# Optimization experiments

Hardware: AMD Instinct MI355X
Metric: run time of the kernel (lower is better)

Reference implementation:

```python
import jax, jax.numpy as jnp
from jax import lax
import numpy as np

T, B, DIN, NQ = 256, 2048, 128, 16  # hidden_dim == n_qubits (required by module math)


def setup_inputs() -> dict:
    key = jax.random.key(0)
    k1, k2, k3 = jax.random.split(key, 3)
    inputs = jax.random.normal(k1, (T, B, DIN), dtype=jnp.float32)
    # stacked params for the 4 gates: forget, input, update, output
    W = jax.random.normal(k2, (4, NQ, DIN + NQ), dtype=jnp.float32) * 0.1
    b = jnp.zeros((4, NQ), dtype=jnp.float32)
    theta = jax.random.normal(k3, (4, NQ), dtype=jnp.float32)
    return {"inputs": inputs, "W": W, "b": b, "theta": theta}


def reference(inputs, W, b, theta):
    # Analytic simulation of each QGate circuit:
    #   RX(x_i) then RX(theta_i) on wire i  ->  product state, <Z_i> = cos(x_i + theta_i)
    #   CNOT chain (0->1, 1->2, ...): Heisenberg picture maps Z_k -> Z_0 Z_1 ... Z_k,
    Tn, Bn, _ = inputs.shape
    nq = theta.shape[-1]
    h0 = jnp.zeros((Bn, nq), dtype=inputs.dtype)
    c0 = jnp.zeros((Bn, nq), dtype=inputs.dtype)

    def step(carry, x):
        hx, cx = carry
        combined = jnp.concatenate([x, hx], axis=1)              # [B, Din+H]
        z = jnp.einsum('bd,gnd->bgn', combined, W) + b           # [B, 4, nq]
        q = jnp.cumprod(jnp.cos(z + theta), axis=-1)             # quantum gate expectations
        f = jax.nn.sigmoid(q[:, 0])
        i = jax.nn.sigmoid(q[:, 1])
        g = jnp.tanh(q[:, 2])
        o = jax.nn.sigmoid(q[:, 3])
        cx = f * cx + i * g
        hx = o * jnp.tanh(cx)
        return (hx, cx), hx

    (hx, cx), outputs = lax.scan(step, (h0, c0), inputs)
    return outputs, hx, cx
```

## Files before the change

kernel.cpp:

```cpp
#include <hip/hip_runtime.h>
#include <hip/hip_bf16.h>
#include <stdint.h>


#define T_STEPS 256
#define BATCH   2048
#define DIN     128
#define NQ      16
#define LCOLS   64
#define DTOT    144
#define NCH     64
#define CH_XSTRIDE ((size_t)4 * BATCH * DIN)

typedef __attribute__((ext_vector_type(8))) short bf16x8;
typedef __attribute__((ext_vector_type(4))) float f32x4;

__device__ __forceinline__ float bf2f(unsigned short u) {
    union { unsigned int i; float f; } v; v.i = ((unsigned int)u) << 16; return v.f;
}
__device__ __forceinline__ unsigned short f2bf(float f) {
    union { float f; unsigned int i; } v; v.f = f;
    unsigned int i = v.i;
    unsigned int r = i + 0x7fffu + ((i >> 16) & 1u);
    return (unsigned short)(r >> 16);
}
__device__ __forceinline__ float ldval(const float* p) { return *p; }
__device__ __forceinline__ float ldval(const unsigned short* p) { return bf2f(*p); }

__device__ __forceinline__ int detect_bf16(const unsigned int* __restrict__ xw, int lane) {
    int cnt = 0;
#pragma unroll
    for (int i = 0; i < 4; ++i) {
        unsigned int w = xw[lane + i * 64];
        unsigned int e = (w >> 7) & 0xFFu;
        cnt += (e >= 100u && e <= 140u) ? 1 : 0;
    }
#pragma unroll
    for (int d = 32; d > 0; d >>= 1) cnt += __shfl_down(cnt, d, 64);
    int tot = __shfl(cnt, 0, 64);
    return (tot >= 140) ? 1 : 0;
}

template <int CTRL>
__device__ __forceinline__ float dpp_sh(float v) {
    int r = __builtin_amdgcn_update_dpp(__builtin_bit_cast(int, 1.0f),
                                        __builtin_bit_cast(int, v),
                                        CTRL, 0xF, 0xF, false);
    return __builtin_bit_cast(float, r);
}
template <int CTRL>
__device__ __forceinline__ float rot16(float v) {
    int r = __builtin_amdgcn_update_dpp(0, __builtin_bit_cast(int, v),
                                        CTRL, 0xF, 0xF, false);
    return __builtin_bit_cast(float, r);
}

template <int BASE>
__device__ __forceinline__ void qstep(int t, int g, int n, float cur,
                                      const float (&Wp)[16], float& h, float& c,
                                      float& hsave, float* __restrict__ out, int b,
                                      int a_f, int a_i, int a_g, int a_o)
{
    float h1  = rot16<0x121>(h), h2  = rot16<0x122>(h), h3  = rot16<0x123>(h);
    float h4  = rot16<0x124>(h), h5  = rot16<0x125>(h), h6  = rot16<0x126>(h), h7  = rot16<0x127>(h);
    float h8  = rot16<0x128>(h), h9  = rot16<0x129>(h), h10 = rot16<0x12A>(h), h11 = rot16<0x12B>(h);
    float h12 = rot16<0x12C>(h), h13 = rot16<0x12D>(h), h14 = rot16<0x12E>(h), h15 = rot16<0x12F>(h);

    float s0 = fmaf(Wp[0],  h,   fmaf(Wp[1],  h1,  fmaf(Wp[2],  h2,  Wp[3]  * h3)));
    float s1 = fmaf(Wp[4],  h4,  fmaf(Wp[5],  h5,  fmaf(Wp[6],  h6,  Wp[7]  * h7)));
    float s2 = fmaf(Wp[8],  h8,  fmaf(Wp[9],  h9,  fmaf(Wp[10], h10, Wp[11] * h11)));
    float s3 = fmaf(Wp[12], h12, fmaf(Wp[13], h13, fmaf(Wp[14], h14, Wp[15] * h15)));
    float z = cur + ((s0 + s1) + (s2 + s3));

    float cz = __cosf(z);
    cz *= dpp_sh<BASE + 1>(cz);
    cz *= dpp_sh<BASE + 2>(cz);
    cz *= dpp_sh<BASE + 4>(cz);
    cz *= dpp_sh<BASE + 8>(cz);

    float a = (g == 2) ? 2.f * cz : cz;
    float e = __expf(-a);
    float rr = __builtin_amdgcn_rcpf(1.f + e);
    float s = (g == 2) ? (1.f - e) * rr : rr;

    int si = __builtin_bit_cast(int, s);
    float fv = __builtin_bit_cast(float, __builtin_amdgcn_ds_bpermute(a_f, si));
    float iv = __builtin_bit_cast(float, __builtin_amdgcn_ds_bpermute(a_i, si));
    float gv = __builtin_bit_cast(float, __builtin_amdgcn_ds_bpermute(a_g, si));
    float ov = __builtin_bit_cast(float, __builtin_amdgcn_ds_bpermute(a_o, si));

    c = fmaf(fv, c, iv * gv);
    float e2 = __expf(-2.f * c);
    float tc = (1.f - e2) * __builtin_amdgcn_rcpf(1.f + e2);
    h = ov * tc;

    if ((t & 3) == g) hsave = h;
    if ((t & 3) == 3)
        out[(size_t)(t - 3 + g) * (BATCH * NQ) + (size_t)b * NQ + n] = hsave;
}

template <int BASE, typename InT>
__device__ __forceinline__ void fused_main(
    const InT* __restrict__ x, const InT* __restrict__ W,
    const InT* __restrict__ bv, const InT* __restrict__ th,
    float* __restrict__ out, int b0, int w, int lane,
    const float (&Wp)[16], float (*zbuf)[16][64], bf16x8* __restrict__ xshv)
{
    const int m = lane & 15, quad = lane >> 4;
    const int g = quad, n = m;
    const int b = b0 + w;
    const int a_f = n << 2, a_i = (16 + n) << 2, a_g = (32 + n) << 2, a_o = (48 + n) << 2;

    bf16x8 bh[4], bl[4];
    if constexpr (sizeof(InT) == 2) {
#pragma unroll
        for (int kt = 0; kt < 4; ++kt)
            bh[kt] = *(const bf16x8*)((const unsigned short*)W +
                                      (size_t)(w * 16 + m) * DTOT + kt * 32 + quad * 8);
    } else {
#pragma unroll
        for (int kt = 0; kt < 4; ++kt) {
            const float* p = (const float*)W + (size_t)(w * 16 + m) * DTOT + kt * 32 + quad * 8;
#pragma unroll
            for (int j = 0; j < 8; ++j) {
                float wv = p[j];
                unsigned short hh = f2bf(wv);
                bh[kt][j] = (short)hh;
                bl[kt][j] = (short)f2bf(wv - bf2f(hh));
            }
        }
    }
    const float bias = ldval(bv + lane) + ldval(th + lane);

    const InT* xbase = x + ((size_t)(m >> 2) * BATCH + (size_t)(b0 + (m & 3))) * DIN
                         + w * 32 + quad * 8;

    bf16x8* xw0 = xshv + (((m * 4 + w) * 4 + quad) * 2);

    f32x4 rx0, rx1; bf16x8 rbx;
    auto LOAD = [&](int ch) {
        const InT* p = xbase + (size_t)ch * CH_XSTRIDE;
        if constexpr (sizeof(InT) == 2) {
            rbx = *(const bf16x8*)p;
        } else {
            rx0 = *(const f32x4*)p;
            rx1 = *(const f32x4*)((const float*)p + 4);
        }
    };
    auto PRODUCE = [&](int ch) {
        if constexpr (sizeof(InT) == 2) {
            xw0[0] = rbx;
        } else {
            bf16x8 ah, al;
#pragma unroll
            for (int j = 0; j < 4; ++j) {
                float xv = rx0[j];
                unsigned short hh = f2bf(xv);
                ah[j] = (short)hh; al[j] = (short)f2bf(xv - bf2f(hh));
            }
#pragma unroll
            for (int j = 0; j < 4; ++j) {
                float xv = rx1[j];
                unsigned short hh = f2bf(xv);
                ah[4 + j] = (short)hh; al[4 + j] = (short)f2bf(xv - bf2f(hh));
            }
            xw0[0] = ah; xw0[1] = al;
        }
        __syncthreads();
        f32x4 acc = {};
#pragma unroll
        for (int kt = 0; kt < 4; ++kt) {
            const bf16x8 ah = xshv[((m * 4 + kt) * 4 + quad) * 2];
            if constexpr (sizeof(InT) == 2) {
                acc = __builtin_amdgcn_mfma_f32_16x16x32_bf16(ah, bh[kt], acc, 0, 0, 0);
            } else {
                const bf16x8 al = xshv[((m * 4 + kt) * 4 + quad) * 2 + 1];
                acc = __builtin_amdgcn_mfma_f32_16x16x32_bf16(ah, bh[kt], acc, 0, 0, 0);
                acc = __builtin_amdgcn_mfma_f32_16x16x32_bf16(al, bh[kt], acc, 0, 0, 0);
                acc = __builtin_amdgcn_mfma_f32_16x16x32_bf16(ah, bl[kt], acc, 0, 0, 0);
            }
        }
        const int buf = ch & 1;
#pragma unroll
        for (int r = 0; r < 4; ++r)
            zbuf[buf][quad * 4 + r][w * 16 + m] = acc[r];
        __syncthreads();
    };

    float h = 0.f, c = 0.f, hsave = 0.f;

    LOAD(0);
    PRODUCE(0);
    LOAD(1);

    for (int ch = 0; ch < NCH; ++ch) {
        float zr[4];
#pragma unroll
        for (int dt = 0; dt < 4; ++dt)
            zr[dt] = zbuf[ch & 1][dt * 4 + w][lane] + bias;
        if (ch < NCH - 1) {
            PRODUCE(ch + 1);
            if (ch + 2 < NCH) LOAD(ch + 2);
        }
#pragma unroll
        for (int dt = 0; dt < 4; ++dt)
            qstep<BASE>(ch * 4 + dt, g, n, zr[dt], Wp, h, c, hsave, out, b,
                        a_f, a_i, a_g, a_o);
    }

    if (g == 0) {
        out[(size_t)T_STEPS * BATCH * NQ + (size_t)b * NQ + n] = h;
        out[(size_t)T_STEPS * BATCH * NQ + (size_t)BATCH * NQ + (size_t)b * NQ + n] = c;
    }
}

__global__ __launch_bounds__(256) void qlstm_fused(
    const void* __restrict__ x_, const void* __restrict__ W_,
    const void* __restrict__ b_, const void* __restrict__ th_,
    float* __restrict__ out)
{
    __shared__ float zbuf[2][16][64];
    __shared__ bf16x8 xshv[512];

    const int lane = threadIdx.x & 63;
    const int w    = threadIdx.x >> 6;
    const int b0   = blockIdx.x * 4;
    const int n    = lane & 15;

    const int isbf = __builtin_amdgcn_readfirstlane(detect_bf16((const unsigned int*)x_, lane));

    int pr  = __builtin_amdgcn_update_dpp(0, lane, 0x121, 0xF, 0xF, false);
    int p0r = __shfl(pr, 0, 64);
    const int d = (p0r == 1) ? 1 : 15;

    float Wp[16];
    if (isbf) {
        const unsigned short* W = (const unsigned short*)W_;
#pragma unroll
        for (int k = 0; k < 16; ++k)
            Wp[k] = bf2f(W[(size_t)lane * DTOT + DIN + ((n + k * d) & 15)]);
    } else {
        const float* W = (const float*)W_;
#pragma unroll
        for (int k = 0; k < 16; ++k)
            Wp[k] = W[(size_t)lane * DTOT + DIN + ((n + k * d) & 15)];
    }

    int probe = __builtin_amdgcn_update_dpp(999, lane, 0x111, 0xF, 0xF, false);
    int p2 = __shfl(probe, 2, 64);

    if (isbf) {
        if (p2 == 1) fused_main<0x110, unsigned short>((const unsigned short*)x_, (const unsigned short*)W_,
                                                       (const unsigned short*)b_, (const unsigned short*)th_,
                                                       out, b0, w, lane, Wp, zbuf, xshv);
        else         fused_main<0x100, unsigned short>((const unsigned short*)x_, (const unsigned short*)W_,
                                                       (const unsigned short*)b_, (const unsigned short*)th_,
                                                       out, b0, w, lane, Wp, zbuf, xshv);
    } else {
        if (p2 == 1) fused_main<0x110, float>((const float*)x_, (const float*)W_,
                                              (const float*)b_, (const float*)th_,
                                              out, b0, w, lane, Wp, zbuf, xshv);
        else         fused_main<0x100, float>((const float*)x_, (const float*)W_,
                                              (const float*)b_, (const float*)th_,
                                              out, b0, w, lane, Wp, zbuf, xshv);
    }
}

extern "C" void kernel_launch(void* const* d_in, const int* in_sizes, int n_in,
                              void* d_out, int out_size, void* d_ws, size_t ws_size,
                              hipStream_t stream) {
    const void* x  = d_in[0];
    const void* W  = d_in[1];
    const void* bv = d_in[2];
    const void* th = d_in[3];
    (void)d_ws; (void)ws_size;
    qlstm_fused<<<BATCH / 4, 256, 0, stream>>>(x, W, bv, th, (float*)d_out);
}
```

Before: 441.7 us.

## Make each wave compute its own 16-step input projection tile without block barriers

Each wave now handles one batch element over 16 timesteps and computes the full 64-column input projection for that tile itself, using 4x4 register-resident weight fragments. Per-wave shared buffers with padded rows replace the block-wide shared staging, so the two __syncthreads per chunk go away. On targets that support it, the gate-value gather uses permlane16/32 swaps instead of four ds_bpermute ops. The cost is much higher register pressure (16 weight fragments, plus low parts for fp32 inputs), and launch bounds now request 2 blocks per CU.

```diff
diff --git a/kernel.cpp b/kernel.cpp
--- a/kernel.cpp
+++ b/kernel.cpp
@@ -9,11 +9,21 @@
 #define NQ      16
 #define LCOLS   64
 #define DTOT    144
-#define NCH     64
-#define CH_XSTRIDE ((size_t)4 * BATCH * DIN)
+#define NTILE   16
+#define ZROW    68
 
 typedef __attribute__((ext_vector_type(8))) short bf16x8;
 typedef __attribute__((ext_vector_type(4))) float f32x4;
+typedef __attribute__((ext_vector_type(2))) int   int2v;
+
+#if defined(__has_builtin)
+#if __has_builtin(__builtin_amdgcn_permlane16_swap) && __has_builtin(__builtin_amdgcn_permlane32_swap)
+#define USE_PLSWAP 1
+#endif
+#endif
+#ifndef USE_PLSWAP
+#define USE_PLSWAP 0
+#endif
 
 __device__ __forceinline__ float bf2f(unsigned short u) {
     union { unsigned int i; float f; } v; v.i = ((unsigned int)u) << 16; return v.f;
@@ -59,6 +69,7 @@
 __device__ __forceinline__ void qstep(int t, int g, int n, float cur,
                                       const float (&Wp)[16], float& h, float& c,
                                       float& hsave, float* __restrict__ out, int b,
+                                      bool m0, bool m1,
                                       int a_f, int a_i, int a_g, int a_o)
 {
     float h1  = rot16<0x121>(h), h2  = rot16<0x122>(h), h3  = rot16<0x123>(h);
@@ -83,15 +94,38 @@
     float rr = __builtin_amdgcn_rcpf(1.f + e);
     float s = (g == 2) ? (1.f - e) * rr : rr;
 
+    float fv, iv, gv, ov;
+#if USE_PLSWAP
     int si = __builtin_bit_cast(int, s);
-    float fv = __builtin_bit_cast(float, __builtin_amdgcn_ds_bpermute(a_f, si));
-    float iv = __builtin_bit_cast(float, __builtin_amdgcn_ds_bpermute(a_i, si));
-    float gv = __builtin_bit_cast(float, __builtin_amdgcn_ds_bpermute(a_g, si));
-    float ov = __builtin_bit_cast(float, __builtin_amdgcn_ds_bpermute(a_o, si));
+    int2v e1 = __builtin_amdgcn_permlane16_swap(si, si, false, false);
+    int c1i = m0 ? e1[0] : e1[1];
+    int2v e2 = __builtin_amdgcn_permlane32_swap(si, si, false, false);
+    int c2i = m1 ? e2[0] : e2[1];
+    int2v e3 = __builtin_amdgcn_permlane16_swap(c2i, c2i, false, false);
+    int c3i = m0 ? e3[0] : e3[1];
+    float C0 = s;
+    float C1 = __builtin_bit_cast(float, c1i);
+    float C2 = __builtin_bit_cast(float, c2i);
+    float C3 = __builtin_bit_cast(float, c3i);
+    float P  = m1 ? C2 : C0;
+    float Q  = m1 ? C3 : C1;
+    float R_ = m1 ? C0 : C2;
+    float S_ = m1 ? C1 : C3;
+    fv = m0 ? Q  : P;
+    iv = m0 ? P  : Q;
+    gv = m0 ? S_ : R_;
+    ov = m0 ? R_ : S_;
+#else
+    int si = __builtin_bit_cast(int, s);
+    fv = __builtin_bit_cast(float, __builtin_amdgcn_ds_bpermute(a_f, si));
+    iv = __builtin_bit_cast(float, __builtin_amdgcn_ds_bpermute(a_i, si));
+    gv = __builtin_bit_cast(float, __builtin_amdgcn_ds_bpermute(a_g, si));
+    ov = __builtin_bit_cast(float, __builtin_amdgcn_ds_bpermute(a_o, si));
+#endif
 
     c = fmaf(fv, c, iv * gv);
-    float e2 = __expf(-2.f * c);
-    float tc = (1.f - e2) * __builtin_amdgcn_rcpf(1.f + e2);
+    float e2t = __expf(-2.f * c);
+    float tc = (1.f - e2t) * __builtin_amdgcn_rcpf(1.f + e2t);
     h = ov * tc;
 
     if ((t & 3) == g) hsave = h;
@@ -103,88 +137,88 @@
 __device__ __forceinline__ void fused_main(
     const InT* __restrict__ x, const InT* __restrict__ W,
     const InT* __restrict__ bv, const InT* __restrict__ th,
-    float* __restrict__ out, int b0, int w, int lane,
-    const float (&Wp)[16], float (*zbuf)[16][64], bf16x8* __restrict__ xshv)
+    float* __restrict__ out, int b, int lane,
+    const float (&Wp)[16], float (*zt)[16][ZROW])
 {
     const int m = lane & 15, quad = lane >> 4;
     const int g = quad, n = m;
-    const int b = b0 + w;
+    const bool m0 = (g & 1) != 0, m1 = (g & 2) != 0;
     const int a_f = n << 2, a_i = (16 + n) << 2, a_g = (32 + n) << 2, a_o = (48 + n) << 2;
 
-    bf16x8 bh[4], bl[4];
+    bf16x8 bh[4][4], bl[4][4];
     if constexpr (sizeof(InT) == 2) {
 #pragma unroll
         for (int kt = 0; kt < 4; ++kt)
-            bh[kt] = *(const bf16x8*)((const unsigned short*)W +
-                                      (size_t)(w * 16 + m) * DTOT + kt * 32 + quad * 8);
+#pragma unroll
+            for (int nb = 0; nb < 4; ++nb)
+                bh[kt][nb] = *(const bf16x8*)((const unsigned short*)W +
+                             (size_t)(nb * 16 + m) * DTOT + kt * 32 + quad * 8);
     } else {
 #pragma unroll
+        for (int kt = 0; kt < 4; ++kt)
+#pragma unroll
+            for (int nb = 0; nb < 4; ++nb) {
+                const float* p = (const float*)W + (size_t)(nb * 16 + m) * DTOT + kt * 32 + quad * 8;
+#pragma unroll
+                for (int j = 0; j < 8; ++j) {
+                    float wv = p[j];
+                    unsigned short hh = f2bf(wv);
+                    bh[kt][nb][j] = (short)hh;
+                    bl[kt][nb][j] = (short)f2bf(wv - bf2f(hh));
+                }
+            }
+    }
+    const float bias = ldval(bv + lane) + ldval(th + lane);
+
+    const InT* xbase = x + ((size_t)m * BATCH + (size_t)b) * DIN + quad * 8;
+
+    f32x4 rx[8]; bf16x8 rbx[4];
+    auto LOAD = [&](int tl) {
+        const InT* p = xbase + (size_t)tl * ((size_t)16 * BATCH * DIN);
+#pragma unroll
         for (int kt = 0; kt < 4; ++kt) {
-            const float* p = (const float*)W + (size_t)(w * 16 + m) * DTOT + kt * 32 + quad * 8;
-#pragma unroll
-            for (int j = 0; j < 8; ++j) {
-                float wv = p[j];
-                unsigned short hh = f2bf(wv);
-                bh[kt][j] = (short)hh;
-                bl[kt][j] = (short)f2bf(wv - bf2f(hh));
+            if constexpr (sizeof(InT) == 2) {
+                rbx[kt] = *(const bf16x8*)(p + kt * 32);
+            } else {
+                rx[2 * kt]     = *(const f32x4*)((const float*)p + kt * 32);
+                rx[2 * kt + 1] = *(const f32x4*)((const float*)p + kt * 32 + 4);
             }
         }
-    }
-    const float bias = ldval(bv + lane) + ldval(th + lane);
-
-    const InT* xbase = x + ((size_t)(m >> 2) * BATCH + (size_t)(b0 + (m & 3))) * DIN
-                         + w * 32 + quad * 8;
-
-    bf16x8* xw0 = xshv + (((m * 4 + w) * 4 + quad) * 2);
-
-    f32x4 rx0, rx1; bf16x8 rbx;
-    auto LOAD = [&](int ch) {
-        const InT* p = xbase + (size_t)ch * CH_XSTRIDE;
-        if constexpr (sizeof(InT) == 2) {
-            rbx = *(const bf16x8*)p;
-        } else {
-            rx0 = *(const f32x4*)p;
-            rx1 = *(const f32x4*)((const float*)p + 4);
-        }
     };
-    auto PRODUCE = [&](int ch) {
-        if constexpr (sizeof(InT) == 2) {
-            xw0[0] = rbx;
-        } else {
-            bf16x8 ah, al;
-#pragma unroll
-            for (int j = 0; j < 4; ++j) {
-                float xv = rx0[j];
-                unsigned short hh = f2bf(xv);
-                ah[j] = (short)hh; al[j] = (short)f2bf(xv - bf2f(hh));
-            }
-#pragma unroll
-            for (int j = 0; j < 4; ++j) {
-                float xv = rx1[j];
-                unsigned short hh = f2bf(xv);
-                ah[4 + j] = (short)hh; al[4 + j] = (short)f2bf(xv - bf2f(hh));
-            }
-            xw0[0] = ah; xw0[1] = al;
-        }
-        __syncthreads();
-        f32x4 acc = {};
+    auto PRODUCE = [&](int tl) {
+        f32x4 acc[4] = {};
 #pragma unroll
         for (int kt = 0; kt < 4; ++kt) {
-            const bf16x8 ah = xshv[((m * 4 + kt) * 4 + quad) * 2];
             if constexpr (sizeof(InT) == 2) {
-                acc = __builtin_amdgcn_mfma_f32_16x16x32_bf16(ah, bh[kt], acc, 0, 0, 0);
+#pragma unroll
+                for (int nb = 0; nb < 4; ++nb)
+                    acc[nb] = __builtin_amdgcn_mfma_f32_16x16x32_bf16(rbx[kt], bh[kt][nb], acc[nb], 0, 0, 0);
             } else {
-                const bf16x8 al = xshv[((m * 4 + kt) * 4 + quad) * 2 + 1];
-                acc = __builtin_amdgcn_mfma_f32_16x16x32_bf16(ah, bh[kt], acc, 0, 0, 0);
-                acc = __builtin_amdgcn_mfma_f32_16x16x32_bf16(al, bh[kt], acc, 0, 0, 0);
-                acc = __builtin_amdgcn_mfma_f32_16x16x32_bf16(ah, bl[kt], acc, 0, 0, 0);
+                bf16x8 ah, al;
+#pragma unroll
+                for (int j = 0; j < 8; ++j) {
+                    float xv = rx[2 * kt + (j >> 2)][j & 3];
+                    unsigned short hh = f2bf(xv);
+                    ah[j] = (short)hh;
+                    al[j] = (short)f2bf(xv - bf2f(hh));
+                }
+#pragma unroll
+                for (int nb = 0; nb < 4; ++nb)
+                    acc[nb] = __builtin_amdgcn_mfma_f32_16x16x32_bf16(ah, bh[kt][nb], acc[nb], 0, 0, 0);
+#pragma unroll
+                for (int nb = 0; nb < 4; ++nb)
+                    acc[nb] = __builtin_amdgcn_mfma_f32_16x16x32_bf16(al, bh[kt][nb], acc[nb], 0, 0, 0);
+#pragma unroll
+                for (int nb = 0; nb < 4; ++nb)
+                    acc[nb] = __builtin_amdgcn_mfma_f32_16x16x32_bf16(ah, bl[kt][nb], acc[nb], 0, 0, 0);
             }
         }
-        const int buf = ch & 1;
-#pragma unroll
-        for (int r = 0; r < 4; ++r)
-            zbuf[buf][quad * 4 + r][w * 16 + m] = acc[r];
-        __syncthreads();
+        const int buf = tl & 1;
+#pragma unroll
+        for (int nb = 0; nb < 4; ++nb)
+#pragma unroll
+            for (int r = 0; r < 4; ++r)
+                zt[buf][quad * 4 + r][nb * 16 + m] = acc[nb][r];
     };
 
     float h = 0.f, c = 0.f, hsave = 0.f;
@@ -193,19 +227,26 @@
     PRODUCE(0);
     LOAD(1);
 
-    for (int ch = 0; ch < NCH; ++ch) {
-        float zr[4];
-#pragma unroll
-        for (int dt = 0; dt < 4; ++dt)
-            zr[dt] = zbuf[ch & 1][dt * 4 + w][lane] + bias;
-        if (ch < NCH - 1) {
-            PRODUCE(ch + 1);
-            if (ch + 2 < NCH) LOAD(ch + 2);
-        }
-#pragma unroll
-        for (int dt = 0; dt < 4; ++dt)
-            qstep<BASE>(ch * 4 + dt, g, n, zr[dt], Wp, h, c, hsave, out, b,
-                        a_f, a_i, a_g, a_o);
+#pragma unroll 1
+    for (int tl = 0; tl < NTILE; ++tl) {
+        const int buf = tl & 1;
+        const int t0 = tl * 16;
+        float zr0[8], zr1[8];
+#pragma unroll
+        for (int j = 0; j < 8; ++j) zr0[j] = zt[buf][j][lane] + bias;
+        if (tl < NTILE - 1) PRODUCE(tl + 1);
+        if (tl < NTILE - 2) LOAD(tl + 2);
+#pragma unroll
+        for (int j = 0; j < 4; ++j)
+            qstep<BASE>(t0 + j, g, n, zr0[j], Wp, h, c, hsave, out, b, m0, m1, a_f, a_i, a_g, a_o);
+#pragma unroll
+        for (int j = 0; j < 8; ++j) zr1[j] = zt[buf][8 + j][lane] + bias;
+#pragma unroll
+        for (int j = 4; j < 8; ++j)
+            qstep<BASE>(t0 + j, g, n, zr0[j], Wp, h, c, hsave, out, b, m0, m1, a_f, a_i, a_g, a_o);
+#pragma unroll
+        for (int j = 0; j < 8; ++j)
+            qstep<BASE>(t0 + 8 + j, g, n, zr1[j], Wp, h, c, hsave, out, b, m0, m1, a_f, a_i, a_g, a_o);
     }
 
     if (g == 0) {
@@ -214,17 +255,16 @@
     }
 }
 
-__global__ __launch_bounds__(256) void qlstm_fused(
+__global__ __launch_bounds__(256, 2) void qlstm_fused(
     const void* __restrict__ x_, const void* __restrict__ W_,
     const void* __restrict__ b_, const void* __restrict__ th_,
     float* __restrict__ out)
 {
-    __shared__ float zbuf[2][16][64];
-    __shared__ bf16x8 xshv[512];
+    __shared__ float zw[4][2][16][ZROW];
 
     const int lane = threadIdx.x & 63;
     const int w    = threadIdx.x >> 6;
-    const int b0   = blockIdx.x * 4;
+    const int b    = blockIdx.x * 4 + w;
     const int n    = lane & 15;
 
     const int isbf = __builtin_amdgcn_readfirstlane(detect_bf16((const unsigned int*)x_, lane));
@@ -252,17 +292,17 @@
     if (isbf) {
         if (p2 == 1) fused_main<0x110, unsigned short>((const unsigned short*)x_, (const unsigned short*)W_,
                                                        (const unsigned short*)b_, (const unsigned short*)th_,
-                                                       out, b0, w, lane, Wp, zbuf, xshv);
+                                                       out, b, lane, Wp, zw[w]);
         else         fused_main<0x100, unsigned short>((const unsigned short*)x_, (const unsigned short*)W_,
                                                        (const unsigned short*)b_, (const unsigned short*)th_,
-                                                       out, b0, w, lane, Wp, zbuf, xshv);
+                                                       out, b, lane, Wp, zw[w]);
     } else {
         if (p2 == 1) fused_main<0x110, float>((const float*)x_, (const float*)W_,
                                               (const float*)b_, (const float*)th_,
-                                              out, b0, w, lane, Wp, zbuf, xshv);
+                                              out, b, lane, Wp, zw[w]);
         else         fused_main<0x100, float>((const float*)x_, (const float*)W_,
                                               (const float*)b_, (const float*)th_,
-                                              out, b0, w, lane, Wp, zbuf, xshv);
+                                              out, b, lane, Wp, zw[w]);
     }
 }
 
```

New measurement: 407.5 us. -7.7%, faster.
